# Kernel tuning notes

Hardware: AMD Instinct MI355X
Metric: run time of the kernel (lower is better)

The kernel has to match this reference:

```python
import jax
import jax.numpy as jnp
from jax import lax
import numpy as np

VOCAB = 50000
EMB = 32
HID = 32
LAYERS = 4
BATCH = 8192
SEQ = 111


def setup_inputs() -> dict:
    key = jax.random.key(0)
    ks = jax.random.split(key, 12)
    s = 0.1
    x = jax.random.randint(ks[0], (BATCH, SEQ), 0, VOCAB, dtype=jnp.int64 if jax.config.read('jax_enable_x64') else jnp.int32)
    emb = jax.random.normal(ks[1], (VOCAB, EMB), jnp.float32) * s
    # stacked per-layer LSTM weights; layer-0 input dim == EMB == HID so stacking is valid
    Wih = jax.random.normal(ks[2], (LAYERS, 4 * HID, EMB), jnp.float32) * s
    Whh = jax.random.normal(ks[3], (LAYERS, 4 * HID, HID), jnp.float32) * s
    bih = jax.random.normal(ks[4], (LAYERS, 4 * HID), jnp.float32) * s
    bhh = jax.random.normal(ks[5], (LAYERS, 4 * HID), jnp.float32) * s
    Wa = jax.random.normal(ks[6], (HID, 1), jnp.float32) * s
    ba = jax.random.normal(ks[7], (1,), jnp.float32) * s
    W1 = jax.random.normal(ks[8], (HID, 32), jnp.float32) * s
    b1 = jax.random.normal(ks[9], (32,), jnp.float32) * s
    W2 = jax.random.normal(ks[10], (32, 3), jnp.float32) * s
    b2 = jax.random.normal(ks[11], (3,), jnp.float32) * s
    return {"x": x, "emb": emb, "Wih": Wih, "Whh": Whh, "bih": bih, "bhh": bhh,
            "Wa": Wa, "ba": ba, "W1": W1, "b1": b1, "W2": W2, "b2": b2}


def _lstm_layer(x, Wih, Whh, bih, bhh):
    # x: [B, T, D] -> [B, T, H]; PyTorch gate order: i, f, g, o
    B = x.shape[0]
    H = Whh.shape[1]
    # precompute the input contribution for all timesteps (one big GEMM)
    xg = jnp.einsum('btd,gd->btg', x, Wih) + bih + bhh  # [B, T, 4H]

    def step(carry, xg_t):
        h, c = carry
        z = xg_t + h @ Whh.T  # [B, 4H]
        i, f, g, o = jnp.split(z, 4, axis=-1)
        c = jax.nn.sigmoid(f) * c + jax.nn.sigmoid(i) * jnp.tanh(g)
        h = jax.nn.sigmoid(o) * jnp.tanh(c)
        return (h, c), h

    init = (jnp.zeros((B, H), x.dtype), jnp.zeros((B, H), x.dtype))
    _, hs = lax.scan(step, init, jnp.swapaxes(xg, 0, 1))  # hs: [T, B, H]
    return jnp.swapaxes(hs, 0, 1)


def reference(x, emb, Wih, Whh, bih, bhh, Wa, ba, W1, b1, W2, b2):
    h = emb[x]  # [B, T, E]
    for l in range(Wih.shape[0]):  # fixed 4 layers
        h = _lstm_layer(h, Wih[l], Whh[l], bih[l], bhh[l])
    scores = h @ Wa + ba                       # [B, T, 1]
    attn = jax.nn.softmax(scores, axis=1)      # softmax over time
    context = jnp.sum(h * attn, axis=1)        # [B, H]
    hid = jnp.tanh(context @ W1 + b1)          # dropout is identity at eval
    return hid @ W2 + b2                       # [B, 3]
```

## Files before the change

### kernel.cpp

```cpp
#include <hip/hip_runtime.h>

#define TSEQ 111
#define L2E 1.44269504088896340736f
#define TWO_L2E 2.88539008177792680472f

using f32x4  = __attribute__((ext_vector_type(4))) float;
using f32x2  = __attribute__((ext_vector_type(2))) float;
using short8 = __attribute__((ext_vector_type(8))) short;

union FragU { unsigned u[4]; uint4 v; short8 s; };

__device__ __forceinline__ float fexp2(float x) { return __builtin_amdgcn_exp2f(x); }
__device__ __forceinline__ float frcp(float x)  { return __builtin_amdgcn_rcpf(x); }
__device__ __forceinline__ float tanh2(float zs) { return 1.f - 2.f * frcp(1.f + fexp2(zs + zs)); }
__device__ __forceinline__ f32x2 exp2v(f32x2 x) { f32x2 r; r[0] = fexp2(x[0]); r[1] = fexp2(x[1]); return r; }
__device__ __forceinline__ f32x2 rcpv(f32x2 x)  { f32x2 r; r[0] = frcp(x[0]); r[1] = frcp(x[1]); return r; }

__device__ __forceinline__ unsigned rnd_bf16(float w) {
  unsigned u = __float_as_uint(w);
  return (u + 0x7fffu + ((u >> 16) & 1u)) >> 16;
}
__device__ __forceinline__ unsigned cvtpk(float a, float b) {
  unsigned r;
  asm("v_cvt_pk_bf16_f32 %0, %1, %2" : "=v"(r) : "v"(a), "v"(b));
  return r;
}

__global__ __launch_bounds__(512, 4) void lstm_fused(
    const int* __restrict__ x, const float* __restrict__ emb,
    const float* __restrict__ Wih, const float* __restrict__ Whh,
    const float* __restrict__ bih, const float* __restrict__ bhh,
    const float* __restrict__ Wa, const float* __restrict__ W1,
    const float* __restrict__ b1, const float* __restrict__ W2,
    const float* __restrict__ b2, float* __restrict__ out)
{
  __shared__ __align__(16) unsigned short hb[2 * 4 * 512];

  const int tid  = threadIdx.x;
  const int wvu  = __builtin_amdgcn_readfirstlane(tid) >> 6;
  const int l    = wvu >> 1;
  const int hf   = wvu & 1;
  const int lane = tid & 63;
  const int c    = lane & 15;
  const int q    = lane >> 4;
  const int gcc  = (c & 3) ^ (c >> 2);
  const int rowbase = blockIdx.x * 16;
  const int xrow = (rowbase + c) * TSEQ;

  const int rdOff = c * 32 + ((q ^ gcc) << 3);
  const int wrOff = c * 32 + ((((2 * hf + (q >> 1)) ^ gcc) << 3) | ((q & 1) << 2));

  FragU wihf[4], whhf[4];
#pragma unroll
  for (int g = 0; g < 4; ++g) {
    const float sj = (g == 2) ? TWO_L2E : -L2E;
    const int wr = 32 * g + 16 * hf + c;
    const float* srcI = Wih + l * 4096 + wr * 32 + 8 * q;
    const float* srcH = Whh + l * 4096 + wr * 32 + 8 * q;
#pragma unroll
    for (int p = 0; p < 4; ++p) {
      wihf[g].u[p] = rnd_bf16(srcI[2 * p] * sj) | (rnd_bf16(srcI[2 * p + 1] * sj) << 16);
      whhf[g].u[p] = rnd_bf16(srcH[2 * p] * sj) | (rnd_bf16(srcH[2 * p + 1] * sj) << 16);
    }
  }
  f32x4 bvv[4];
#pragma unroll
  for (int g = 0; g < 4; ++g) {
    const float sj = (g == 2) ? TWO_L2E : -L2E;
    const int bi = l * 128 + 32 * g + 16 * hf + 4 * q;
#pragma unroll
    for (int e = 0; e < 4; ++e)
      bvv[g][e] = (bih[bi + e] + bhh[bi + e]) * sj;
  }

  FragU wahA, walA;
#pragma unroll
  for (int p = 0; p < 4; ++p) { wahA.u[p] = 0u; walA.u[p] = 0u; }
  if (l == 3) {
#pragma unroll
    for (int p = 0; p < 4; ++p) {
      const int k0 = 8 * q + 2 * p;
      float w0 = Wa[k0] * L2E, w1 = Wa[k0 + 1] * L2E;
      unsigned h0 = rnd_bf16(w0), h1b = rnd_bf16(w1);
      wahA.u[p] = h0 | (h1b << 16);
      float l0v = w0 - __uint_as_float(h0 << 16);
      float l1v = w1 - __uint_as_float(h1b << 16);
      walA.u[p] = rnd_bf16(l0v) | (rnd_bf16(l1v) << 16);
    }
  }

  f32x2 cs2[2];
  cs2[0] = (f32x2){0.f, 0.f}; cs2[1] = (f32x2){0.f, 0.f};
  float mr = -1e30f, sr = 0.f, cx[4];
#pragma unroll
  for (int e = 0; e < 4; ++e) cx[e] = 0.f;

  for (int i = tid; i < 2 * 4 * 512 / 2; i += 512) ((unsigned*)hb)[i] = 0u;

  float4 emA = make_float4(0.f, 0.f, 0.f, 0.f), emB = emA;
  int idxn = 0;
  if (l == 0) {
    int i0 = x[xrow];
    emA = *(const float4*)(emb + i0 * 32 + 8 * q);
    emB = *(const float4*)(emb + i0 * 32 + 8 * q + 4);
    idxn = x[xrow + 1];
  }
  __syncthreads();

#pragma unroll 2
  for (int s = 0; s < TSEQ + 4; ++s) {
    const int t = s - l;
    const bool active = ((unsigned)t < (unsigned)TSEQ);
    const int rp = (s + 1) & 1;
    const int wp = s & 1;
    const bool doAtt = (l == 3) && (s >= 4);

    FragU fi, fh;
    __builtin_amdgcn_s_setprio(1);
    if (active) {
      if (l == 0) {
        fi.u[0] = cvtpk(emA.x, emA.y); fi.u[1] = cvtpk(emA.z, emA.w);
        fi.u[2] = cvtpk(emB.x, emB.y); fi.u[3] = cvtpk(emB.z, emB.w);
        if (t + 1 < TSEQ) {
          emA = *(const float4*)(emb + idxn * 32 + 8 * q);
          emB = *(const float4*)(emb + idxn * 32 + 8 * q + 4);
        }
        if (t + 2 < TSEQ) idxn = x[xrow + t + 2];
      } else {
        fi.v = *(const uint4*)(hb + (rp * 4 + (l - 1)) * 512 + rdOff);
      }
    }
    if (active || doAtt)
      fh.v = *(const uint4*)(hb + (rp * 4 + l) * 512 + rdOff);

    f32x4 acc[4];
    if (active) {
#pragma unroll
      for (int g = 0; g < 4; ++g) {
        acc[g] = __builtin_amdgcn_mfma_f32_16x16x32_bf16(wihf[g].s, fi.s, bvv[g], 0, 0, 0);
        acc[g] = __builtin_amdgcn_mfma_f32_16x16x32_bf16(whhf[g].s, fh.s, acc[g], 0, 0, 0);
      }
    }
    f32x4 sacc;
    if (doAtt) {
      f32x4 z = {0.f, 0.f, 0.f, 0.f};
      sacc = __builtin_amdgcn_mfma_f32_16x16x32_bf16(wahA.s, fh.s, z, 0, 0, 0);
      sacc = __builtin_amdgcn_mfma_f32_16x16x32_bf16(walA.s, fh.s, sacc, 0, 0, 0);
    }
    __builtin_amdgcn_s_setprio(0);

    if (active) {
      float hv[4];
      const f32x2 one = {1.f, 1.f};
      const f32x2 tl2 = {TWO_L2E, TWO_L2E};
#pragma unroll
      for (int pr2 = 0; pr2 < 2; ++pr2) {
        const int e0 = 2 * pr2;
        f32x2 va; va[0] = acc[0][e0]; va[1] = acc[0][e0 + 1];
        f32x2 vm; vm[0] = acc[1][e0]; vm[1] = acc[1][e0 + 1];
        f32x2 vb; vb[0] = acc[2][e0]; vb[1] = acc[2][e0 + 1];
        f32x2 vp; vp[0] = acc[3][e0]; vp[1] = acc[3][e0 + 1];
        f32x2 ea = exp2v(va), em_ = exp2v(vm), eb = exp2v(vb), ep = exp2v(vp);
        f32x2 P  = (one + ea) * (one + eb);
        f32x2 M1 = one + em_;
        f32x2 num = cs2[pr2] * P + (eb - one) * M1;
        f32x2 cn = num * rcpv(M1 * P);
        cs2[pr2] = cn;
        f32x2 qa = cn * tl2;
        qa[0] = fminf(qa[0], 80.f); qa[1] = fminf(qa[1], 80.f);
        f32x2 qv = exp2v(qa);
        f32x2 hvv = (qv - one) * rcpv((one + ep) * (one + qv));
        hv[e0] = hvv[0]; hv[e0 + 1] = hvv[1];
      }

      *(uint2*)(hb + (wp * 4 + l) * 512 + wrOff) =
          make_uint2(cvtpk(hv[0], hv[1]), cvtpk(hv[2], hv[3]));
    }

    asm volatile("s_waitcnt lgkmcnt(0)\n\ts_barrier" ::: "memory");

    if (doAtt) {
      float pf = sacc[0];
      float mn = fmaxf(mr, pf);
      float sc = fexp2(mr - mn);
      float pr = fexp2(pf - mn);
      sr = sr * sc + pr;
#pragma unroll
      for (int p = 0; p < 2; ++p) {
        unsigned w = fh.u[2 * hf + p];
        cx[2 * p]     = cx[2 * p]     * sc + pr * __uint_as_float(w << 16);
        cx[2 * p + 1] = cx[2 * p + 1] * sc + pr * __uint_as_float(w & 0xffff0000u);
      }
      mr = mn;
    }
  }

  __syncthreads();

  float* cb = (float*)hb;
  if (l == 3) {
    float inv = frcp(sr);
#pragma unroll
    for (int e = 0; e < 4; ++e)
      cb[c * 33 + 8 * q + 4 * hf + e] = cx[e] * inv;
  }
  __syncthreads();
  if (wvu != 6) return;

  float a0[4], a1[4];
  {
    float bb0 = b1[c], bb1 = b1[c + 16];
#pragma unroll
    for (int e = 0; e < 4; ++e) { a0[e] = bb0; a1[e] = bb1; }
    for (int j = 0; j < 32; ++j) {
      float w0 = W1[j * 32 + c];
      float w1 = W1[j * 32 + c + 16];
#pragma unroll
      for (int e = 0; e < 4; ++e) {
        float cr = cb[(4 * q + e) * 33 + j];
        a0[e] = fmaf(cr, w0, a0[e]);
        a1[e] = fmaf(cr, w1, a1[e]);
      }
    }
  }
  float o0[4], o1[4], o2[4];
  {
    float w20 = W2[c * 3 + 0], w21 = W2[c * 3 + 1], w22 = W2[c * 3 + 2];
    float w30 = W2[(c + 16) * 3 + 0], w31 = W2[(c + 16) * 3 + 1], w32 = W2[(c + 16) * 3 + 2];
#pragma unroll
    for (int e = 0; e < 4; ++e) {
      float h0 = tanh2(a0[e] * L2E);
      float hB = tanh2(a1[e] * L2E);
      o0[e] = h0 * w20 + hB * w30;
      o1[e] = h0 * w21 + hB * w31;
      o2[e] = h0 * w22 + hB * w32;
    }
  }
#pragma unroll
  for (int mk = 1; mk <= 8; mk <<= 1) {
#pragma unroll
    for (int e = 0; e < 4; ++e) {
      o0[e] += __shfl_xor(o0[e], mk, 64);
      o1[e] += __shfl_xor(o1[e], mk, 64);
      o2[e] += __shfl_xor(o2[e], mk, 64);
    }
  }
  if (c < 3) {
    float bb = b2[c];
#pragma unroll
    for (int e = 0; e < 4; ++e) {
      float v = (c == 0) ? o0[e] : ((c == 1) ? o1[e] : o2[e]);
      out[(rowbase + 4 * q + e) * 3 + c] = v + bb;
    }
  }
}

extern "C" void kernel_launch(void* const* d_in, const int* in_sizes, int n_in,
                              void* d_out, int out_size, void* d_ws, size_t ws_size,
                              hipStream_t stream) {
  const int*   x   = (const int*)d_in[0];
  const float* emb = (const float*)d_in[1];
  const float* Wih = (const float*)d_in[2];
  const float* Whh = (const float*)d_in[3];
  const float* bih = (const float*)d_in[4];
  const float* bhh = (const float*)d_in[5];
  const float* Wa  = (const float*)d_in[6];
  const float* W1  = (const float*)d_in[8];
  const float* b1  = (const float*)d_in[9];
  const float* W2  = (const float*)d_in[10];
  const float* b2  = (const float*)d_in[11];
  float* out = (float*)d_out;

  lstm_fused<<<512, 512, 0, stream>>>(x, emb, Wih, Whh, bih, bhh, Wa, W1, b1, W2, b2, out);
}
```

Before: 158.6 us.

## Split each LSTM layer across four waves with gate-interleaved MFMA rows

Doubles the block to 1024 threads so each layer gets four wavefronts instead of two. Weight rows are permuted so that each MFMA output tile holds all four gates of two hidden units, which cuts per-wave MFMAs from eight to four and activation math to one pair per lane. Attention accumulation now uses the previous step's fp32 hidden values kept in registers instead of unpacking bf16 from LDS. The embedding prefetch reuses the attention weight registers to save VGPRs. In exchange, the 512-thread barrier per timestep becomes a 1024-thread barrier, and occupancy pressure rises under the 1024,8 launch bounds.

```diff
diff --git a/kernel.cpp b/kernel.cpp
--- a/kernel.cpp
+++ b/kernel.cpp
@@ -25,8 +25,9 @@
   asm("v_cvt_pk_bf16_f32 %0, %1, %2" : "=v"(r) : "v"(a), "v"(b));
   return r;
 }
-
-__global__ __launch_bounds__(512, 4) void lstm_fused(
+__device__ __forceinline__ float uaf(unsigned u) { return __uint_as_float(u); }
+
+__global__ __launch_bounds__(1024, 8) void lstm_fused(
     const int* __restrict__ x, const float* __restrict__ emb,
     const float* __restrict__ Wih, const float* __restrict__ Whh,
     const float* __restrict__ bih, const float* __restrict__ bhh,
@@ -38,8 +39,8 @@
 
   const int tid  = threadIdx.x;
   const int wvu  = __builtin_amdgcn_readfirstlane(tid) >> 6;
-  const int l    = wvu >> 1;
-  const int hf   = wvu & 1;
+  const int l    = wvu >> 2;
+  const int uq   = wvu & 3;
   const int lane = tid & 63;
   const int c    = lane & 15;
   const int q    = lane >> 4;
@@ -48,63 +49,57 @@
   const int xrow = (rowbase + c) * TSEQ;
 
   const int rdOff = c * 32 + ((q ^ gcc) << 3);
-  const int wrOff = c * 32 + ((((2 * hf + (q >> 1)) ^ gcc) << 3) | ((q & 1) << 2));
-
-  FragU wihf[4], whhf[4];
-#pragma unroll
-  for (int g = 0; g < 4; ++g) {
-    const float sj = (g == 2) ? TWO_L2E : -L2E;
-    const int wr = 32 * g + 16 * hf + c;
-    const float* srcI = Wih + l * 4096 + wr * 32 + 8 * q;
-    const float* srcH = Whh + l * 4096 + wr * 32 + 8 * q;
+  const int wrOff = c * 32 + ((uq ^ gcc) << 3) + 2 * q;
+
+  FragU wif[2], whf[2];
+  f32x4 bvv[2];
+#pragma unroll
+  for (int t = 0; t < 2; ++t) {
+    const int gate = c & 3;
+    const float sj = (gate == 2) ? TWO_L2E : -L2E;
+    const int unit = 8 * uq + 2 * (c >> 2) + t;
+    const float* srcI = Wih + l * 4096 + (32 * gate + unit) * 32 + 8 * q;
+    const float* srcH = Whh + l * 4096 + (32 * gate + unit) * 32 + 8 * q;
 #pragma unroll
     for (int p = 0; p < 4; ++p) {
-      wihf[g].u[p] = rnd_bf16(srcI[2 * p] * sj) | (rnd_bf16(srcI[2 * p + 1] * sj) << 16);
-      whhf[g].u[p] = rnd_bf16(srcH[2 * p] * sj) | (rnd_bf16(srcH[2 * p + 1] * sj) << 16);
-    }
-  }
-  f32x4 bvv[4];
-#pragma unroll
-  for (int g = 0; g < 4; ++g) {
-    const float sj = (g == 2) ? TWO_L2E : -L2E;
-    const int bi = l * 128 + 32 * g + 16 * hf + 4 * q;
-#pragma unroll
-    for (int e = 0; e < 4; ++e)
-      bvv[g][e] = (bih[bi + e] + bhh[bi + e]) * sj;
-  }
-
-  FragU wahA, walA;
-#pragma unroll
-  for (int p = 0; p < 4; ++p) { wahA.u[p] = 0u; walA.u[p] = 0u; }
+      wif[t].u[p] = rnd_bf16(srcI[2 * p] * sj) | (rnd_bf16(srcI[2 * p + 1] * sj) << 16);
+      whf[t].u[p] = rnd_bf16(srcH[2 * p] * sj) | (rnd_bf16(srcH[2 * p + 1] * sj) << 16);
+    }
+#pragma unroll
+    for (int e = 0; e < 4; ++e) {
+      const float se = (e == 2) ? TWO_L2E : -L2E;
+      const int bi = l * 128 + 32 * e + 8 * uq + 2 * q + t;
+      bvv[t][e] = (bih[bi] + bhh[bi]) * se;
+    }
+  }
+
+  FragU xA, xB;
+#pragma unroll
+  for (int p = 0; p < 4; ++p) { xA.u[p] = 0u; xB.u[p] = 0u; }
+  int idxn = 0;
+  if (l == 0) {
+    int i0 = x[xrow];
+    xA.v = *(const uint4*)(emb + i0 * 32 + 8 * q);
+    xB.v = *(const uint4*)(emb + i0 * 32 + 8 * q + 4);
+    idxn = x[xrow + 1];
+  }
   if (l == 3) {
 #pragma unroll
     for (int p = 0; p < 4; ++p) {
       const int k0 = 8 * q + 2 * p;
       float w0 = Wa[k0] * L2E, w1 = Wa[k0 + 1] * L2E;
       unsigned h0 = rnd_bf16(w0), h1b = rnd_bf16(w1);
-      wahA.u[p] = h0 | (h1b << 16);
+      xA.u[p] = h0 | (h1b << 16);
       float l0v = w0 - __uint_as_float(h0 << 16);
       float l1v = w1 - __uint_as_float(h1b << 16);
-      walA.u[p] = rnd_bf16(l0v) | (rnd_bf16(l1v) << 16);
-    }
-  }
-
-  f32x2 cs2[2];
-  cs2[0] = (f32x2){0.f, 0.f}; cs2[1] = (f32x2){0.f, 0.f};
-  float mr = -1e30f, sr = 0.f, cx[4];
-#pragma unroll
-  for (int e = 0; e < 4; ++e) cx[e] = 0.f;
-
-  for (int i = tid; i < 2 * 4 * 512 / 2; i += 512) ((unsigned*)hb)[i] = 0u;
-
-  float4 emA = make_float4(0.f, 0.f, 0.f, 0.f), emB = emA;
-  int idxn = 0;
-  if (l == 0) {
-    int i0 = x[xrow];
-    emA = *(const float4*)(emb + i0 * 32 + 8 * q);
-    emB = *(const float4*)(emb + i0 * 32 + 8 * q + 4);
-    idxn = x[xrow + 1];
-  }
+      xB.u[p] = rnd_bf16(l0v) | (rnd_bf16(l1v) << 16);
+    }
+  }
+
+  f32x2 cs = {0.f, 0.f}, cx = {0.f, 0.f}, hvPrev = {0.f, 0.f};
+  float mr = -1e30f, sr = 0.f;
+
+  for (int i = tid; i < 2 * 4 * 512 / 2; i += 1024) ((unsigned*)hb)[i] = 0u;
   __syncthreads();
 
 #pragma unroll 2
@@ -119,11 +114,13 @@
     __builtin_amdgcn_s_setprio(1);
     if (active) {
       if (l == 0) {
-        fi.u[0] = cvtpk(emA.x, emA.y); fi.u[1] = cvtpk(emA.z, emA.w);
-        fi.u[2] = cvtpk(emB.x, emB.y); fi.u[3] = cvtpk(emB.z, emB.w);
+        fi.u[0] = cvtpk(uaf(xA.u[0]), uaf(xA.u[1]));
+        fi.u[1] = cvtpk(uaf(xA.u[2]), uaf(xA.u[3]));
+        fi.u[2] = cvtpk(uaf(xB.u[0]), uaf(xB.u[1]));
+        fi.u[3] = cvtpk(uaf(xB.u[2]), uaf(xB.u[3]));
         if (t + 1 < TSEQ) {
-          emA = *(const float4*)(emb + idxn * 32 + 8 * q);
-          emB = *(const float4*)(emb + idxn * 32 + 8 * q + 4);
+          xA.v = *(const uint4*)(emb + idxn * 32 + 8 * q);
+          xB.v = *(const uint4*)(emb + idxn * 32 + 8 * q + 4);
         }
         if (t + 2 < TSEQ) idxn = x[xrow + t + 2];
       } else {
@@ -133,51 +130,20 @@
     if (active || doAtt)
       fh.v = *(const uint4*)(hb + (rp * 4 + l) * 512 + rdOff);
 
-    f32x4 acc[4];
+    f32x4 acc0, acc1;
     if (active) {
-#pragma unroll
-      for (int g = 0; g < 4; ++g) {
-        acc[g] = __builtin_amdgcn_mfma_f32_16x16x32_bf16(wihf[g].s, fi.s, bvv[g], 0, 0, 0);
-        acc[g] = __builtin_amdgcn_mfma_f32_16x16x32_bf16(whhf[g].s, fh.s, acc[g], 0, 0, 0);
-      }
+      acc0 = __builtin_amdgcn_mfma_f32_16x16x32_bf16(wif[0].s, fi.s, bvv[0], 0, 0, 0);
+      acc0 = __builtin_amdgcn_mfma_f32_16x16x32_bf16(whf[0].s, fh.s, acc0, 0, 0, 0);
+      acc1 = __builtin_amdgcn_mfma_f32_16x16x32_bf16(wif[1].s, fi.s, bvv[1], 0, 0, 0);
+      acc1 = __builtin_amdgcn_mfma_f32_16x16x32_bf16(whf[1].s, fh.s, acc1, 0, 0, 0);
     }
     f32x4 sacc;
     if (doAtt) {
       f32x4 z = {0.f, 0.f, 0.f, 0.f};
-      sacc = __builtin_amdgcn_mfma_f32_16x16x32_bf16(wahA.s, fh.s, z, 0, 0, 0);
-      sacc = __builtin_amdgcn_mfma_f32_16x16x32_bf16(walA.s, fh.s, sacc, 0, 0, 0);
+      sacc = __builtin_amdgcn_mfma_f32_16x16x32_bf16(xA.s, fh.s, z, 0, 0, 0);
+      sacc = __builtin_amdgcn_mfma_f32_16x16x32_bf16(xB.s, fh.s, sacc, 0, 0, 0);
     }
     __builtin_amdgcn_s_setprio(0);
-
-    if (active) {
-      float hv[4];
-      const f32x2 one = {1.f, 1.f};
-      const f32x2 tl2 = {TWO_L2E, TWO_L2E};
-#pragma unroll
-      for (int pr2 = 0; pr2 < 2; ++pr2) {
-        const int e0 = 2 * pr2;
-        f32x2 va; va[0] = acc[0][e0]; va[1] = acc[0][e0 + 1];
-        f32x2 vm; vm[0] = acc[1][e0]; vm[1] = acc[1][e0 + 1];
-        f32x2 vb; vb[0] = acc[2][e0]; vb[1] = acc[2][e0 + 1];
-        f32x2 vp; vp[0] = acc[3][e0]; vp[1] = acc[3][e0 + 1];
-        f32x2 ea = exp2v(va), em_ = exp2v(vm), eb = exp2v(vb), ep = exp2v(vp);
-        f32x2 P  = (one + ea) * (one + eb);
-        f32x2 M1 = one + em_;
-        f32x2 num = cs2[pr2] * P + (eb - one) * M1;
-        f32x2 cn = num * rcpv(M1 * P);
-        cs2[pr2] = cn;
-        f32x2 qa = cn * tl2;
-        qa[0] = fminf(qa[0], 80.f); qa[1] = fminf(qa[1], 80.f);
-        f32x2 qv = exp2v(qa);
-        f32x2 hvv = (qv - one) * rcpv((one + ep) * (one + qv));
-        hv[e0] = hvv[0]; hv[e0 + 1] = hvv[1];
-      }
-
-      *(uint2*)(hb + (wp * 4 + l) * 512 + wrOff) =
-          make_uint2(cvtpk(hv[0], hv[1]), cvtpk(hv[2], hv[3]));
-    }
-
-    asm volatile("s_waitcnt lgkmcnt(0)\n\ts_barrier" ::: "memory");
 
     if (doAtt) {
       float pf = sacc[0];
@@ -185,14 +151,32 @@
       float sc = fexp2(mr - mn);
       float pr = fexp2(pf - mn);
       sr = sr * sc + pr;
-#pragma unroll
-      for (int p = 0; p < 2; ++p) {
-        unsigned w = fh.u[2 * hf + p];
-        cx[2 * p]     = cx[2 * p]     * sc + pr * __uint_as_float(w << 16);
-        cx[2 * p + 1] = cx[2 * p + 1] * sc + pr * __uint_as_float(w & 0xffff0000u);
-      }
+      cx[0] = cx[0] * sc + pr * hvPrev[0];
+      cx[1] = cx[1] * sc + pr * hvPrev[1];
       mr = mn;
     }
+
+    if (active) {
+      f32x2 va; va[0] = acc0[0]; va[1] = acc1[0];
+      f32x2 vm; vm[0] = acc0[1]; vm[1] = acc1[1];
+      f32x2 vb; vb[0] = acc0[2]; vb[1] = acc1[2];
+      f32x2 vp; vp[0] = acc0[3]; vp[1] = acc1[3];
+      const f32x2 one = {1.f, 1.f};
+      f32x2 ea = exp2v(va), em_ = exp2v(vm), eb = exp2v(vb), ep = exp2v(vp);
+      f32x2 P  = (one + ea) * (one + eb);
+      f32x2 M1 = one + em_;
+      f32x2 cn = (cs * P + (eb - one) * M1) * rcpv(M1 * P);
+      cs = cn;
+      f32x2 qa; qa[0] = fminf(cn[0] * TWO_L2E, 80.f); qa[1] = fminf(cn[1] * TWO_L2E, 80.f);
+      f32x2 qv = exp2v(qa);
+      f32x2 hvv = (qv - one) * rcpv((one + ep) * (one + qv));
+
+      *(unsigned*)(hb + (wp * 4 + l) * 512 + wrOff) = cvtpk(hvv[0], hvv[1]);
+
+      if (l == 3) hvPrev = hvv;
+    }
+
+    asm volatile("s_waitcnt lgkmcnt(0)\n\ts_barrier" ::: "memory");
   }
 
   __syncthreads();
@@ -200,9 +184,8 @@
   float* cb = (float*)hb;
   if (l == 3) {
     float inv = frcp(sr);
-#pragma unroll
-    for (int e = 0; e < 4; ++e)
-      cb[c * 33 + 8 * q + 4 * hf + e] = cx[e] * inv;
+    cb[c * 33 + 8 * uq + 2 * q]     = cx[0] * inv;
+    cb[c * 33 + 8 * uq + 2 * q + 1] = cx[1] * inv;
   }
   __syncthreads();
   if (wvu != 6) return;
@@ -271,5 +254,5 @@
   const float* b2  = (const float*)d_in[11];
   float* out = (float*)d_out;
 
-  lstm_fused<<<512, 512, 0, stream>>>(x, emb, Wih, Whh, bih, bhh, Wa, W1, b1, W2, b2, out);
-}
+  lstm_fused<<<512, 1024, 0, stream>>>(x, emb, Wih, Whh, bih, bhh, Wa, W1, b1, W2, b2, out);
+}
```

After: 326.3 us. 106% more time.
